# Optimization experiments

Hardware: AMD Instinct MI355X
Metric: run time of the kernel (lower is better)

The kernel has to match this reference:

```python
import jax, jax.numpy as jnp
import numpy as np
from jax import lax

B, S, H = 8, 2048, 1024


def setup_inputs() -> dict:
    key = jax.random.key(0)
    ks = jax.random.split(key, 4)
    x = jax.random.normal(ks[0], (B, S, H), dtype=jnp.float32)
    # torch Linear(H, 3H, bias=False): weight [3H, H]; store transposed [H, 3H]
    W = jax.random.normal(ks[1], (H, 3 * H), dtype=jnp.float32) / np.sqrt(H)
    vf = jax.random.normal(ks[2], (H,), dtype=jnp.float32)
    vr = jax.random.normal(ks[3], (H,), dtype=jnp.float32)
    bf = jnp.zeros((H,), dtype=jnp.float32)
    br = jnp.zeros((H,), dtype=jnp.float32)
    return {"x": x, "W": W, "vf": vf, "vr": vr, "bf": bf, "br": br}


def reference(x, W, vf, vr, bf, br):
    # projection: [B,S,H] @ [H,3H] -> [B,S,3H]
    ux = jnp.einsum('bsh,hk->bsk', x, W)
    xf, xc, xr = jnp.split(ux, 3, axis=-1)
    xf = xf + bf
    xr = xr + br

    def step(ct, ins):
        xt, xft, xct, xrt = ins
        ft = jax.nn.sigmoid(xft + vf * ct)
        rt = jax.nn.sigmoid(xrt + vr * ct)
        c = ft * ct + (1.0 - ft) * xct
        ht = rt * c + (1.0 - rt) * xt
        return c, ht

    # scan over time: move seq dim to front -> [S,B,H]
    xs = tuple(jnp.swapaxes(a, 0, 1) for a in (x, xf, xc, xr))
    c0 = jnp.zeros((x.shape[0], x.shape[2]), dtype=x.dtype)
    cfinal, ys = lax.scan(step, c0, xs)
    y = jnp.swapaxes(ys, 0, 1)  # [B,S,H]
    return y, cfinal
```

## Files before the change

kernel.cpp:

```cpp
#include <hip/hip_runtime.h>
#include <cstdint>
#include <cstddef>

#define B_   8
#define S_   2048
#define H_   1024
#define K3_  3072
#define SC_  512
#define TB_  (SC_ / 4)
#define WSCALE 32.0f

typedef __attribute__((ext_vector_type(8))) _Float16 f16x8;
typedef __attribute__((ext_vector_type(4))) _Float16 f16x4;
typedef __attribute__((ext_vector_type(4))) float f32x4;


__device__ __forceinline__ void cast_body(const float4* __restrict__ X,
                                          f16x4* __restrict__ Xh, f16x4* __restrict__ Xl,
                                          int ci, int tid, int s0) {
    const int nthr = (B_ * SC_ * H_) >> 4;
    int i0 = ci * 256 + tid;
#pragma unroll
    for (int u = 0; u < 4; ++u) {
        int i  = i0 + u * nthr;
        int r  = i >> 8;
        int c4 = i & 255;
        int b  = r >> 9;
        int sl = r & (SC_ - 1);
        size_t src = ((size_t)b * S_ + s0 + sl) * (H_ / 4) + c4;
        float4 v = X[src];
        _Float16 h0 = (_Float16)v.x, h1 = (_Float16)v.y, h2 = (_Float16)v.z, h3 = (_Float16)v.w;
        f16x4 hv = {h0, h1, h2, h3};
        f16x4 lv = {(_Float16)(v.x - (float)h0), (_Float16)(v.y - (float)h1),
                    (_Float16)(v.z - (float)h2), (_Float16)(v.w - (float)h3)};
        size_t dst = ((size_t)b * SC_ + sl) * (H_ / 4) + c4;
        Xh[dst] = hv;
        Xl[dst] = lv;
    }
}

__device__ __forceinline__ void xpose_body(const float* __restrict__ X, float* __restrict__ X4,
                                           int ci, int tid, int s0, float (*tile)[33]) {
    int tx = tid & 31, ty = tid >> 5;
#pragma unroll
    for (int it = 0; it < 4; ++it) {
        int tg   = ci * 4 + it;
        int b    = tg >> 9;
        int tt   = tg & 511;
        int tb32 = tt >> 5;
        int hb   = tt & 31;
#pragma unroll
        for (int i2 = 0; i2 < 4; ++i2) {
            int t = tb32 * 32 + ty + i2 * 8;
            tile[ty + i2 * 8][tx] = X[((size_t)b * S_ + s0 + t) * H_ + hb * 32 + tx];
        }
        __syncthreads();
        int h  = hb * 32 + tx;
        int tb = tb32 * 8 + ty;
        float4 v = {tile[ty * 4 + 0][tx], tile[ty * 4 + 1][tx],
                    tile[ty * 4 + 2][tx], tile[ty * 4 + 3][tx]};
        *(float4*)(X4 + ((size_t)(b * TB_ + tb) * H_ + h) * 4) = v;
        __syncthreads();
    }
}

__global__ __launch_bounds__(256) void castx_kernel(const float4* __restrict__ X,
                                                    f16x4* __restrict__ Xh,
                                                    f16x4* __restrict__ Xl, int s0) {
    cast_body(X, Xh, Xl, blockIdx.x, threadIdx.x, s0);
}

__global__ __launch_bounds__(256) void xpose_kernel(const float* __restrict__ X,
                                                    float* __restrict__ X4, int s0) {
    __shared__ float tile[32][33];
    xpose_body(X, X4, blockIdx.x, threadIdx.x, s0, tile);
}

__global__ __launch_bounds__(256) void prep_kernel(const float* __restrict__ W,
                                                   _Float16* __restrict__ Wth,
                                                   _Float16* __restrict__ Wtl,
                                                   const float4* __restrict__ X,
                                                   f16x4* __restrict__ Xh,
                                                   f16x4* __restrict__ Xl) {
    __shared__ float tile[32][33];
    if ((int)blockIdx.x < 3072) {
        int idx = blockIdx.x;
        int bc  = (idx % 96) * 32;
        int brr = (idx / 96) * 32;
        int tx = threadIdx.x & 31;
        int ty = threadIdx.x >> 5;
#pragma unroll
        for (int i = 0; i < 4; ++i) {
            int r = ty + i * 8;
            tile[r][tx] = W[(size_t)(brr + r) * K3_ + bc + tx];
        }
        __syncthreads();
#pragma unroll
        for (int i = 0; i < 4; ++i) {
            int r = ty + i * 8;
            float v = tile[tx][r] * WSCALE;
            _Float16 h = (_Float16)v;
            _Float16 l = (_Float16)(v - (float)h);
            Wth[(size_t)(bc + r) * H_ + brr + tx] = h;
            Wtl[(size_t)(bc + r) * H_ + brr + tx] = l;
        }
    } else {
        cast_body(X, Xh, Xl, (int)blockIdx.x - 3072, threadIdx.x, 0);
    }
}

__global__ __launch_bounds__(256) void fused_kernel(
        const _Float16* __restrict__ Ah, const _Float16* __restrict__ Al,
        const _Float16* __restrict__ Bh, const _Float16* __restrict__ Bl,
        float* __restrict__ C, int nGemm,
        const float* __restrict__ Uprev, int s0scan, int nScan,
        const float* __restrict__ X,
        f16x4* __restrict__ Xch, f16x4* __restrict__ Xcl, int s0cast,
        float* __restrict__ Xt4, int xtMode,
        const float* __restrict__ vf,  const float* __restrict__ vr,
        const float* __restrict__ bfv, const float* __restrict__ brv,
        float* __restrict__ Y, float* __restrict__ carry) {
    __shared__ _Float16 Ahs[128 * 32];
    __shared__ _Float16 Als[128 * 32];
    __shared__ _Float16 Bhs[128 * 32];
    __shared__ _Float16 Bls[128 * 32];

    if ((int)blockIdx.x < nScan) {
        int gid = blockIdx.x * 256 + threadIdx.x;
        int b = gid >> 10;
        int h = gid & 1023;
        float vfh = vf[h], vrh = vr[h], bfh = bfv[h], brh = brv[h];
        const float* Ub4 = Uprev + ((size_t)(b * TB_) * K3_ + h) * 4;
        const float* Xb = X + ((size_t)b * S_ + s0scan) * H_ + h;
        float* Yb = Y + ((size_t)b * S_ + s0scan) * H_ + h;
        float c = (s0scan == 0) ? 0.f : carry[gid];

        float Af[8], Ac[8], Ar[8], Ax[8];
        float Bf[8], Bc[8], Br[8], Bx[8];
        auto LOAD = [&](int t0, float (&sf)[8], float (&sc)[8], float (&sr)[8], float (&sx)[8]) {
#pragma unroll
            for (int q = 0; q < 2; ++q) {
                const float* up = Ub4 + (size_t)((t0 >> 2) + q) * (K3_ * 4);
                float4 a  = *(const float4*)(up);
                float4 bb = *(const float4*)(up + H_ * 4);
                float4 cc = *(const float4*)(up + 2 * H_ * 4);
                sf[q*4+0]=a.x;  sf[q*4+1]=a.y;  sf[q*4+2]=a.z;  sf[q*4+3]=a.w;
                sc[q*4+0]=bb.x; sc[q*4+1]=bb.y; sc[q*4+2]=bb.z; sc[q*4+3]=bb.w;
                sr[q*4+0]=cc.x; sr[q*4+1]=cc.y; sr[q*4+2]=cc.z; sr[q*4+3]=cc.w;
            }
#pragma unroll
            for (int u = 0; u < 8; ++u) sx[u] = Xb[(size_t)(t0 + u) * H_];
        };
        auto COMP = [&](int t0, float (&sf)[8], float (&sc)[8], float (&sr)[8], float (&sx)[8]) {
#pragma unroll
            for (int u = 0; u < 8; ++u) {
                float zf = sf[u] + bfh + vfh * c;
                float zr = sr[u] + brh + vrh * c;
                float xc = sc[u];
                float ft = __builtin_amdgcn_rcpf(1.f + __expf(-zf));
                float rt = __builtin_amdgcn_rcpf(1.f + __expf(-zr));
                c = ft * (c - xc) + xc;
                float xv = sx[u];
                float ht = rt * (c - xv) + xv;
                Yb[(size_t)(t0 + u) * H_] = ht;
            }
        };
        LOAD(0, Af, Ac, Ar, Ax);
        for (int t0 = 0; t0 < SC_; t0 += 16) {
            LOAD(t0 + 8, Bf, Bc, Br, Bx);
            COMP(t0, Af, Ac, Ar, Ax);
            if (t0 + 16 < SC_) LOAD(t0 + 16, Af, Ac, Ar, Ax);
            COMP(t0 + 8, Bf, Bc, Br, Bx);
        }
        carry[gid] = c;
        return;
    }

    if ((int)blockIdx.x >= nScan + nGemm) {
        int ci = (int)blockIdx.x - nScan - nGemm;
        if (xtMode) xpose_body(X, Xt4, ci, threadIdx.x, s0cast, (float (*)[33])Ahs);
        else        cast_body((const float4*)X, Xch, Xcl, ci, threadIdx.x, s0cast);
        return;
    }

    const int idxg = (int)blockIdx.x - nScan;
    const int bm   = (idxg / 24) * 128;
    const int bn   = (idxg % 24) * 128;
    const int tid  = threadIdx.x;
    const int lane = tid & 63;
    const int w    = tid >> 6;
    const int wm   = (w >> 1) * 64;
    const int wn   = (w & 1) * 64;
    const int K    = 1024;

    f32x4 acc[4][4];
#pragma unroll
    for (int i = 0; i < 4; ++i)
#pragma unroll
        for (int j = 0; j < 4; ++j) {
            f32x4 z = {0.f, 0.f, 0.f, 0.f};
            acc[i][j] = z;
        }

    const int quad = lane >> 4;
    const int lrow = lane & 15;

    for (int kk = 0; kk < K; kk += 32) {
#pragma unroll
        for (int j = 0; j < 2; ++j) {
            int idx = j * 256 + tid;
            int row = idx >> 2;
            int kp  = (((idx & 3) ^ ((row >> 1) & 3)) << 3);
            size_t aoff = (size_t)(bm + row) * K + kk + kp;
            size_t boff = (size_t)(bn + row) * K + kk + kp;
            unsigned base = (unsigned)(j * 256 + (tid & ~63)) * 16u;
            __builtin_amdgcn_global_load_lds(
                (const __attribute__((address_space(1))) void*)(Ah + aoff),
                (__attribute__((address_space(3))) void*)((char*)Ahs + base), 16, 0, 0);
            __builtin_amdgcn_global_load_lds(
                (const __attribute__((address_space(1))) void*)(Al + aoff),
                (__attribute__((address_space(3))) void*)((char*)Als + base), 16, 0, 0);
            __builtin_amdgcn_global_load_lds(
                (const __attribute__((address_space(1))) void*)(Bh + boff),
                (__attribute__((address_space(3))) void*)((char*)Bhs + base), 16, 0, 0);
            __builtin_amdgcn_global_load_lds(
                (const __attribute__((address_space(1))) void*)(Bl + boff),
                (__attribute__((address_space(3))) void*)((char*)Bls + base), 16, 0, 0);
        }
        __syncthreads();

        f16x8 ah[4], al[4], bh[4], bl[4];
#pragma unroll
        for (int i = 0; i < 4; ++i) {
            int r = wm + i * 16 + lrow;
            unsigned off = (unsigned)r * 64u + (unsigned)((quad ^ ((r >> 1) & 3)) << 4);
            ah[i] = *(const f16x8*)((const char*)Ahs + off);
            al[i] = *(const f16x8*)((const char*)Als + off);
        }
#pragma unroll
        for (int j = 0; j < 4; ++j) {
            int r = wn + j * 16 + lrow;
            unsigned off = (unsigned)r * 64u + (unsigned)((quad ^ ((r >> 1) & 3)) << 4);
            bh[j] = *(const f16x8*)((const char*)Bhs + off);
            bl[j] = *(const f16x8*)((const char*)Bls + off);
        }

#pragma unroll
        for (int i = 0; i < 4; ++i)
#pragma unroll
            for (int j = 0; j < 4; ++j) {
                acc[i][j] = __builtin_amdgcn_mfma_f32_16x16x32_f16(al[i], bh[j], acc[i][j], 0, 0, 0);
                acc[i][j] = __builtin_amdgcn_mfma_f32_16x16x32_f16(ah[i], bl[j], acc[i][j], 0, 0, 0);
                acc[i][j] = __builtin_amdgcn_mfma_f32_16x16x32_f16(ah[i], bh[j], acc[i][j], 0, 0, 0);
            }
        __syncthreads();
    }

    const float inv = 1.0f / WSCALE;
#pragma unroll
    for (int i = 0; i < 4; ++i)
#pragma unroll
        for (int j = 0; j < 4; ++j) {
            int row = bm + wm + i * 16 + quad * 4;
            int col = bn + wn + j * 16 + lrow;
            float4 v = {acc[i][j][0] * inv, acc[i][j][1] * inv,
                        acc[i][j][2] * inv, acc[i][j][3] * inv};
            *(float4*)(C + ((size_t)(row >> 2) * K3_ + col) * 4) = v;
        }
}

__global__ __launch_bounds__(64, 1) void scan_final_kernel(const float* __restrict__ U4,
                                                           const float* __restrict__ X4,
                                                           const float* __restrict__ vf,
                                                           const float* __restrict__ vr,
                                                           const float* __restrict__ bfv,
                                                           const float* __restrict__ brv,
                                                           float* __restrict__ Y,
                                                           float* __restrict__ Cf,
                                                           const float* __restrict__ carry,
                                                           int s0) {
    int lane = threadIdx.x;
    if (lane >= 32) return;
    int gid = blockIdx.x * 32 + lane;
    int b = gid >> 10;
    int h = gid & 1023;
    float vfh = vf[h], vrh = vr[h], bfh = bfv[h], brh = brv[h];
    const float* Ub4 = U4 + ((size_t)(b * TB_) * K3_ + h) * 4;
    const float* Xb4 = X4 + ((size_t)(b * TB_) * H_ + h) * 4;
    float* Yb = Y + ((size_t)b * S_ + s0) * H_ + h;
    float c = carry[gid];

    float Af[8], Ac[8], Ar[8], Ax[8];
    float Bf[8], Bc[8], Br[8], Bx[8];
    float Cg[8], Cc[8], Cr[8], Cx[8];
    float Df[8], Dc[8], Dr[8], Dx[8];

    auto LOAD = [&](int t0, float (&sf)[8], float (&sc)[8], float (&sr)[8], float (&sx)[8]) {
#pragma unroll
        for (int q = 0; q < 2; ++q) {
            size_t tb = (size_t)((t0 >> 2) + q);
            const float* up = Ub4 + tb * (K3_ * 4);
            float4 a  = *(const float4*)(up);
            float4 bb = *(const float4*)(up + H_ * 4);
            float4 cc = *(const float4*)(up + 2 * H_ * 4);
            float4 xx = *(const float4*)(Xb4 + tb * (H_ * 4));
            sf[q*4+0]=a.x;  sf[q*4+1]=a.y;  sf[q*4+2]=a.z;  sf[q*4+3]=a.w;
            sc[q*4+0]=bb.x; sc[q*4+1]=bb.y; sc[q*4+2]=bb.z; sc[q*4+3]=bb.w;
            sr[q*4+0]=cc.x; sr[q*4+1]=cc.y; sr[q*4+2]=cc.z; sr[q*4+3]=cc.w;
            sx[q*4+0]=xx.x; sx[q*4+1]=xx.y; sx[q*4+2]=xx.z; sx[q*4+3]=xx.w;
        }
    };
    auto COMP = [&](int t0, float (&sf)[8], float (&sc)[8], float (&sr)[8], float (&sx)[8]) {
#pragma unroll
        for (int u = 0; u < 8; ++u) {
            float zf = sf[u] + bfh + vfh * c;
            float zr = sr[u] + brh + vrh * c;
            float xc = sc[u];
            float ft = __builtin_amdgcn_rcpf(1.f + __expf(-zf));
            float rt = __builtin_amdgcn_rcpf(1.f + __expf(-zr));
            c = ft * (c - xc) + xc;
            float xv = sx[u];
            float ht = rt * (c - xv) + xv;
            Yb[(size_t)(t0 + u) * H_] = ht;
        }
    };

    LOAD(0, Af, Ac, Ar, Ax);
    LOAD(8, Bf, Bc, Br, Bx);
    LOAD(16, Cg, Cc, Cr, Cx);
    for (int t0 = 0; t0 < SC_; t0 += 32) {
        LOAD(t0 + 24, Df, Dc, Dr, Dx);
        COMP(t0, Af, Ac, Ar, Ax);
        if (t0 + 32 < SC_) LOAD(t0 + 32, Af, Ac, Ar, Ax);
        COMP(t0 + 8, Bf, Bc, Br, Bx);
        if (t0 + 40 < SC_) LOAD(t0 + 40, Bf, Bc, Br, Bx);
        COMP(t0 + 16, Cg, Cc, Cr, Cx);
        if (t0 + 48 < SC_) LOAD(t0 + 48, Cg, Cc, Cr, Cx);
        COMP(t0 + 24, Df, Dc, Dr, Dx);
    }
    Cf[(size_t)b * H_ + h] = c;
}

extern "C" void kernel_launch(void* const* d_in, const int* in_sizes, int n_in,
                              void* d_out, int out_size, void* d_ws, size_t ws_size,
                              hipStream_t stream) {
    const float* x  = (const float*)d_in[0];
    const float* W  = (const float*)d_in[1];
    const float* vf = (const float*)d_in[2];
    const float* vr = (const float*)d_in[3];
    const float* bf = (const float*)d_in[4];
    const float* br = (const float*)d_in[5];
    float* y  = (float*)d_out;
    float* cf = y + (size_t)B_ * S_ * H_;

    char* base = (char*)d_ws;
    float* U0 = (float*)base;
    float* U1 = (float*)(base + 50331648);
    _Float16* xh0 = (_Float16*)(base + 100663296);
    _Float16* xl0 = (_Float16*)(base + 109051904);
    _Float16* Wth = (_Float16*)(base + 117440512);
    _Float16* Wtl = (_Float16*)(base + 123731968);
    float* carry  = (float*)(base + 130023424);
    _Float16* xh1 = (_Float16*)(base + 130056192);
    _Float16* xl1 = (_Float16*)(base + 138444800);
    float* Xt4    = (float*)(base + 100663296);

    const bool big = ws_size >= 146833408ULL;
    float* Ubuf[2] = {U0, U1};
    _Float16* Xh[2] = {xh0, big ? xh1 : xh0};
    _Float16* Xl[2] = {xl0, big ? xl1 : xl0};

    prep_kernel<<<3072 + 1024, 256, 0, stream>>>(W, Wth, Wtl, (const float4*)x,
                                                 (f16x4*)xh0, (f16x4*)xl0);

    const int NGEMM = (B_ * SC_ / 128) * 24;
    for (int i = 0; i < 4; ++i) {
        const int nScan = (i >= 1) ? 32 : 0;
        int nCast = 0, s0C = 0, nxt = i, xtM = 0;
        if (big) {
            nCast = 1024;
            if (i < 3) { nxt = i + 1; s0C = (i + 1) * SC_; }
            else       { s0C = 3 * SC_; xtM = 1; }
        } else if (i >= 1) {
            castx_kernel<<<1024, 256, 0, stream>>>((const float4*)x, (f16x4*)xh0,
                                                   (f16x4*)xl0, i * SC_);
        }
        const _Float16* Ahp = Xh[big ? (i & 1) : 0];
        const _Float16* Alp = Xl[big ? (i & 1) : 0];
        fused_kernel<<<nScan + NGEMM + nCast, 256, 0, stream>>>(
            Ahp, Alp, Wth, Wtl, Ubuf[i & 1], NGEMM,
            (i >= 1) ? Ubuf[(i - 1) & 1] : Ubuf[0],
            (i >= 1) ? (i - 1) * SC_ : 0, nScan,
            x, (f16x4*)Xh[nxt & 1], (f16x4*)Xl[nxt & 1], s0C,
            Xt4, xtM, vf, vr, bf, br, y, carry);
    }

    if (!big) xpose_kernel<<<1024, 256, 0, stream>>>(x, Xt4, 3 * SC_);

    scan_final_kernel<<<256, 64, 0, stream>>>(Ubuf[1], Xt4, vf, vr, bf, br, y, cf, carry, 3 * SC_);
}
```

Baseline: 544.8 us.

## Enlarge GEMM tiles to 256x256 with double-buffered LDS and drop x transpose

The fused GEMM moves from 128x128 tiles with 256 threads to 256x256 tiles with 512 threads. It double-buffers the LDS staging, using explicit vmcnt waits and barriers in place of two syncthreads per k-step. The cast blocks are cut to 32 larger blocks, and the final-chunk x transpose is removed, so the last scan reads x directly with strided scalar loads. This aims for more data reuse per tile and overlap of loads with MFMA, at the cost of 128KB of LDS, only 192 GEMM blocks for the whole GPU, and uncoalesced-in-time x reads in the final scan.

```diff
diff --git a/kernel.cpp b/kernel.cpp
--- a/kernel.cpp
+++ b/kernel.cpp
@@ -9,6 +9,7 @@
 #define SC_  512
 #define TB_  (SC_ / 4)
 #define WSCALE 32.0f
+#define NGEMM_ 192
 
 typedef __attribute__((ext_vector_type(8))) _Float16 f16x8;
 typedef __attribute__((ext_vector_type(4))) _Float16 f16x4;
@@ -39,41 +40,10 @@
     }
 }
 
-__device__ __forceinline__ void xpose_body(const float* __restrict__ X, float* __restrict__ X4,
-                                           int ci, int tid, int s0, float (*tile)[33]) {
-    int tx = tid & 31, ty = tid >> 5;
-#pragma unroll
-    for (int it = 0; it < 4; ++it) {
-        int tg   = ci * 4 + it;
-        int b    = tg >> 9;
-        int tt   = tg & 511;
-        int tb32 = tt >> 5;
-        int hb   = tt & 31;
-#pragma unroll
-        for (int i2 = 0; i2 < 4; ++i2) {
-            int t = tb32 * 32 + ty + i2 * 8;
-            tile[ty + i2 * 8][tx] = X[((size_t)b * S_ + s0 + t) * H_ + hb * 32 + tx];
-        }
-        __syncthreads();
-        int h  = hb * 32 + tx;
-        int tb = tb32 * 8 + ty;
-        float4 v = {tile[ty * 4 + 0][tx], tile[ty * 4 + 1][tx],
-                    tile[ty * 4 + 2][tx], tile[ty * 4 + 3][tx]};
-        *(float4*)(X4 + ((size_t)(b * TB_ + tb) * H_ + h) * 4) = v;
-        __syncthreads();
-    }
-}
-
 __global__ __launch_bounds__(256) void castx_kernel(const float4* __restrict__ X,
                                                     f16x4* __restrict__ Xh,
                                                     f16x4* __restrict__ Xl, int s0) {
     cast_body(X, Xh, Xl, blockIdx.x, threadIdx.x, s0);
-}
-
-__global__ __launch_bounds__(256) void xpose_kernel(const float* __restrict__ X,
-                                                    float* __restrict__ X4, int s0) {
-    __shared__ float tile[32][33];
-    xpose_body(X, X4, blockIdx.x, threadIdx.x, s0, tile);
 }
 
 __global__ __launch_bounds__(256) void prep_kernel(const float* __restrict__ W,
@@ -109,24 +79,23 @@
     }
 }
 
-__global__ __launch_bounds__(256) void fused_kernel(
+__global__ __launch_bounds__(512, 2) void fused_kernel(
         const _Float16* __restrict__ Ah, const _Float16* __restrict__ Al,
         const _Float16* __restrict__ Bh, const _Float16* __restrict__ Bl,
         float* __restrict__ C, int nGemm,
         const float* __restrict__ Uprev, int s0scan, int nScan,
         const float* __restrict__ X,
         f16x4* __restrict__ Xch, f16x4* __restrict__ Xcl, int s0cast,
-        float* __restrict__ Xt4, int xtMode,
         const float* __restrict__ vf,  const float* __restrict__ vr,
         const float* __restrict__ bfv, const float* __restrict__ brv,
         float* __restrict__ Y, float* __restrict__ carry) {
-    __shared__ _Float16 Ahs[128 * 32];
-    __shared__ _Float16 Als[128 * 32];
-    __shared__ _Float16 Bhs[128 * 32];
-    __shared__ _Float16 Bls[128 * 32];
+    __shared__ _Float16 SH[2][4][256 * 32];
+
+    const int tid = threadIdx.x;
 
     if ((int)blockIdx.x < nScan) {
-        int gid = blockIdx.x * 256 + threadIdx.x;
+        if (tid >= 256) return;
+        int gid = blockIdx.x * 256 + tid;
         int b = gid >> 10;
         int h = gid & 1023;
         float vfh = vf[h], vrh = vr[h], bfh = bfv[h], brh = brv[h];
@@ -177,88 +146,123 @@
     }
 
     if ((int)blockIdx.x >= nScan + nGemm) {
+        if (s0cast < 0) return;
         int ci = (int)blockIdx.x - nScan - nGemm;
-        if (xtMode) xpose_body(X, Xt4, ci, threadIdx.x, s0cast, (float (*)[33])Ahs);
-        else        cast_body((const float4*)X, Xch, Xcl, ci, threadIdx.x, s0cast);
+        const float4* X4p = (const float4*)X;
+        int gid0 = ci * 512 + tid;
+#pragma unroll 4
+        for (int u = 0; u < 64; ++u) {
+            int i  = gid0 + u * 16384;
+            int r  = i >> 8;
+            int c4 = i & 255;
+            int b  = r >> 9;
+            int sl = r & (SC_ - 1);
+            float4 v = X4p[((size_t)b * S_ + s0cast + sl) * (H_ / 4) + c4];
+            _Float16 h0 = (_Float16)v.x, h1 = (_Float16)v.y, h2 = (_Float16)v.z, h3 = (_Float16)v.w;
+            f16x4 hv = {h0, h1, h2, h3};
+            f16x4 lv = {(_Float16)(v.x - (float)h0), (_Float16)(v.y - (float)h1),
+                        (_Float16)(v.z - (float)h2), (_Float16)(v.w - (float)h3)};
+            size_t dst = ((size_t)b * SC_ + sl) * (H_ / 4) + c4;
+            Xch[dst] = hv;
+            Xcl[dst] = lv;
+        }
         return;
     }
 
     const int idxg = (int)blockIdx.x - nScan;
-    const int bm   = (idxg / 24) * 128;
-    const int bn   = (idxg % 24) * 128;
-    const int tid  = threadIdx.x;
+    const int bm   = (idxg / 12) * 256;
+    const int bn   = (idxg % 12) * 256;
     const int lane = tid & 63;
     const int w    = tid >> 6;
-    const int wm   = (w >> 1) * 64;
-    const int wn   = (w & 1) * 64;
+    const int wm   = (w >> 2) * 128;
+    const int wn   = (w & 3) * 64;
     const int K    = 1024;
 
-    f32x4 acc[4][4];
-#pragma unroll
-    for (int i = 0; i < 4; ++i)
+    const int quad = lane >> 4;
+    const int lrow = lane & 15;
+
+    f32x4 acc[8][4];
+#pragma unroll
+    for (int i = 0; i < 8; ++i)
 #pragma unroll
         for (int j = 0; j < 4; ++j) {
             f32x4 z = {0.f, 0.f, 0.f, 0.f};
             acc[i][j] = z;
         }
 
-    const int quad = lane >> 4;
-    const int lrow = lane & 15;
-
-    for (int kk = 0; kk < K; kk += 32) {
+    auto STAGE = [&](int kt, int bi) {
+        int kk = kt * 32;
 #pragma unroll
         for (int j = 0; j < 2; ++j) {
-            int idx = j * 256 + tid;
+            int idx = j * 512 + tid;
             int row = idx >> 2;
             int kp  = (((idx & 3) ^ ((row >> 1) & 3)) << 3);
             size_t aoff = (size_t)(bm + row) * K + kk + kp;
             size_t boff = (size_t)(bn + row) * K + kk + kp;
-            unsigned base = (unsigned)(j * 256 + (tid & ~63)) * 16u;
+            unsigned base = (unsigned)(j * 512 + (tid & ~63)) * 16u;
             __builtin_amdgcn_global_load_lds(
                 (const __attribute__((address_space(1))) void*)(Ah + aoff),
-                (__attribute__((address_space(3))) void*)((char*)Ahs + base), 16, 0, 0);
+                (__attribute__((address_space(3))) void*)((char*)&SH[bi][0][0] + base), 16, 0, 0);
             __builtin_amdgcn_global_load_lds(
                 (const __attribute__((address_space(1))) void*)(Al + aoff),
-                (__attribute__((address_space(3))) void*)((char*)Als + base), 16, 0, 0);
+                (__attribute__((address_space(3))) void*)((char*)&SH[bi][1][0] + base), 16, 0, 0);
             __builtin_amdgcn_global_load_lds(
                 (const __attribute__((address_space(1))) void*)(Bh + boff),
-                (__attribute__((address_space(3))) void*)((char*)Bhs + base), 16, 0, 0);
+                (__attribute__((address_space(3))) void*)((char*)&SH[bi][2][0] + base), 16, 0, 0);
             __builtin_amdgcn_global_load_lds(
                 (const __attribute__((address_space(1))) void*)(Bl + boff),
-                (__attribute__((address_space(3))) void*)((char*)Bls + base), 16, 0, 0);
-        }
-        __syncthreads();
-
-        f16x8 ah[4], al[4], bh[4], bl[4];
-#pragma unroll
-        for (int i = 0; i < 4; ++i) {
-            int r = wm + i * 16 + lrow;
-            unsigned off = (unsigned)r * 64u + (unsigned)((quad ^ ((r >> 1) & 3)) << 4);
-            ah[i] = *(const f16x8*)((const char*)Ahs + off);
-            al[i] = *(const f16x8*)((const char*)Als + off);
-        }
+                (__attribute__((address_space(3))) void*)((char*)&SH[bi][3][0] + base), 16, 0, 0);
+        }
+    };
+
+    auto COMPUTE = [&](int bi) {
+        const char* pAh = (const char*)&SH[bi][0][0];
+        const char* pAl = (const char*)&SH[bi][1][0];
+        const char* pBh = (const char*)&SH[bi][2][0];
+        const char* pBl = (const char*)&SH[bi][3][0];
+        f16x8 bhf[4], blf[4];
 #pragma unroll
         for (int j = 0; j < 4; ++j) {
             int r = wn + j * 16 + lrow;
             unsigned off = (unsigned)r * 64u + (unsigned)((quad ^ ((r >> 1) & 3)) << 4);
-            bh[j] = *(const f16x8*)((const char*)Bhs + off);
-            bl[j] = *(const f16x8*)((const char*)Bls + off);
-        }
-
-#pragma unroll
-        for (int i = 0; i < 4; ++i)
+            bhf[j] = *(const f16x8*)(pBh + off);
+            blf[j] = *(const f16x8*)(pBl + off);
+        }
+#pragma unroll
+        for (int i = 0; i < 8; ++i) {
+            int r = wm + i * 16 + lrow;
+            unsigned off = (unsigned)r * 64u + (unsigned)((quad ^ ((r >> 1) & 3)) << 4);
+            f16x8 a_h = *(const f16x8*)(pAh + off);
+            f16x8 a_l = *(const f16x8*)(pAl + off);
 #pragma unroll
             for (int j = 0; j < 4; ++j) {
-                acc[i][j] = __builtin_amdgcn_mfma_f32_16x16x32_f16(al[i], bh[j], acc[i][j], 0, 0, 0);
-                acc[i][j] = __builtin_amdgcn_mfma_f32_16x16x32_f16(ah[i], bl[j], acc[i][j], 0, 0, 0);
-                acc[i][j] = __builtin_amdgcn_mfma_f32_16x16x32_f16(ah[i], bh[j], acc[i][j], 0, 0, 0);
+                acc[i][j] = __builtin_amdgcn_mfma_f32_16x16x32_f16(a_l, bhf[j], acc[i][j], 0, 0, 0);
+                acc[i][j] = __builtin_amdgcn_mfma_f32_16x16x32_f16(a_h, blf[j], acc[i][j], 0, 0, 0);
+                acc[i][j] = __builtin_amdgcn_mfma_f32_16x16x32_f16(a_h, bhf[j], acc[i][j], 0, 0, 0);
             }
-        __syncthreads();
-    }
+        }
+    };
+
+    STAGE(0, 0);
+    STAGE(1, 1);
+    for (int t = 0; t < 31; ++t) {
+        asm volatile("s_waitcnt vmcnt(8)" ::: "memory");
+        __builtin_amdgcn_s_barrier();
+        __builtin_amdgcn_sched_barrier(0);
+        COMPUTE(t & 1);
+        __builtin_amdgcn_sched_barrier(0);
+        __builtin_amdgcn_s_barrier();
+        __builtin_amdgcn_sched_barrier(0);
+        if (t < 30) STAGE(t + 2, t & 1);
+    }
+    asm volatile("s_waitcnt vmcnt(0)" ::: "memory");
+    __builtin_amdgcn_s_barrier();
+    __builtin_amdgcn_sched_barrier(0);
+    COMPUTE(1);
 
     const float inv = 1.0f / WSCALE;
 #pragma unroll
-    for (int i = 0; i < 4; ++i)
+    for (int i = 0; i < 8; ++i)
 #pragma unroll
         for (int j = 0; j < 4; ++j) {
             int row = bm + wm + i * 16 + quad * 4;
@@ -270,7 +274,7 @@
 }
 
 __global__ __launch_bounds__(64, 1) void scan_final_kernel(const float* __restrict__ U4,
-                                                           const float* __restrict__ X4,
+                                                           const float* __restrict__ X,
                                                            const float* __restrict__ vf,
                                                            const float* __restrict__ vr,
                                                            const float* __restrict__ bfv,
@@ -286,7 +290,7 @@
     int h = gid & 1023;
     float vfh = vf[h], vrh = vr[h], bfh = bfv[h], brh = brv[h];
     const float* Ub4 = U4 + ((size_t)(b * TB_) * K3_ + h) * 4;
-    const float* Xb4 = X4 + ((size_t)(b * TB_) * H_ + h) * 4;
+    const float* Xb = X + ((size_t)b * S_ + s0) * H_ + h;
     float* Yb = Y + ((size_t)b * S_ + s0) * H_ + h;
     float c = carry[gid];
 
@@ -303,12 +307,12 @@
             float4 a  = *(const float4*)(up);
             float4 bb = *(const float4*)(up + H_ * 4);
             float4 cc = *(const float4*)(up + 2 * H_ * 4);
-            float4 xx = *(const float4*)(Xb4 + tb * (H_ * 4));
             sf[q*4+0]=a.x;  sf[q*4+1]=a.y;  sf[q*4+2]=a.z;  sf[q*4+3]=a.w;
             sc[q*4+0]=bb.x; sc[q*4+1]=bb.y; sc[q*4+2]=bb.z; sc[q*4+3]=bb.w;
             sr[q*4+0]=cc.x; sr[q*4+1]=cc.y; sr[q*4+2]=cc.z; sr[q*4+3]=cc.w;
-            sx[q*4+0]=xx.x; sx[q*4+1]=xx.y; sx[q*4+2]=xx.z; sx[q*4+3]=xx.w;
-        }
+        }
+#pragma unroll
+        for (int u = 0; u < 8; ++u) sx[u] = Xb[(size_t)(t0 + u) * H_];
     };
     auto COMP = [&](int t0, float (&sf)[8], float (&sc)[8], float (&sr)[8], float (&sx)[8]) {
 #pragma unroll
@@ -363,7 +367,6 @@
     float* carry  = (float*)(base + 130023424);
     _Float16* xh1 = (_Float16*)(base + 130056192);
     _Float16* xl1 = (_Float16*)(base + 138444800);
-    float* Xt4    = (float*)(base + 100663296);
 
     const bool big = ws_size >= 146833408ULL;
     float* Ubuf[2] = {U0, U1};
@@ -373,29 +376,26 @@
     prep_kernel<<<3072 + 1024, 256, 0, stream>>>(W, Wth, Wtl, (const float4*)x,
                                                  (f16x4*)xh0, (f16x4*)xl0);
 
-    const int NGEMM = (B_ * SC_ / 128) * 24;
     for (int i = 0; i < 4; ++i) {
         const int nScan = (i >= 1) ? 32 : 0;
-        int nCast = 0, s0C = 0, nxt = i, xtM = 0;
-        if (big) {
-            nCast = 1024;
-            if (i < 3) { nxt = i + 1; s0C = (i + 1) * SC_; }
-            else       { s0C = 3 * SC_; xtM = 1; }
-        } else if (i >= 1) {
+        int nCast = 0, s0C = -1, nxt = i;
+        if (big && i < 3) {
+            nxt   = i + 1;
+            nCast = 32;
+            s0C   = nxt * SC_;
+        } else if (!big && i >= 1) {
             castx_kernel<<<1024, 256, 0, stream>>>((const float4*)x, (f16x4*)xh0,
                                                    (f16x4*)xl0, i * SC_);
         }
         const _Float16* Ahp = Xh[big ? (i & 1) : 0];
         const _Float16* Alp = Xl[big ? (i & 1) : 0];
-        fused_kernel<<<nScan + NGEMM + nCast, 256, 0, stream>>>(
-            Ahp, Alp, Wth, Wtl, Ubuf[i & 1], NGEMM,
+        fused_kernel<<<nScan + NGEMM_ + nCast, 512, 0, stream>>>(
+            Ahp, Alp, Wth, Wtl, Ubuf[i & 1], NGEMM_,
             (i >= 1) ? Ubuf[(i - 1) & 1] : Ubuf[0],
             (i >= 1) ? (i - 1) * SC_ : 0, nScan,
             x, (f16x4*)Xh[nxt & 1], (f16x4*)Xl[nxt & 1], s0C,
-            Xt4, xtM, vf, vr, bf, br, y, carry);
-    }
-
-    if (!big) xpose_kernel<<<1024, 256, 0, stream>>>(x, Xt4, 3 * SC_);
-
-    scan_final_kernel<<<256, 64, 0, stream>>>(Ubuf[1], Xt4, vf, vr, bf, br, y, cf, carry, 3 * SC_);
-}
+            vf, vr, bf, br, y, carry);
+    }
+
+    scan_final_kernel<<<256, 64, 0, stream>>>(Ubuf[1], x, vf, vr, bf, br, y, cf, carry, 3 * SC_);
+}
```

Result: faster. 486.6 us (-10.7%).
